# Optimization experiments

Measured on AMD Instinct MI355X. Metric: run time of the kernel, lower is better.

The kernel has to match this reference:

```python
import jax, jax.numpy as jnp
import numpy as np

N_NODES = 50000
N_EDGES = 800000
C = 128
NEG_SLOPE = 0.01  # nn.LeakyReLU default


def _init_linear(key, fan_in, fan_out):
    kw, kb = jax.random.split(key)
    lim = 1.0 / np.sqrt(fan_in)
    W = jax.random.uniform(kw, (fan_in, fan_out), jnp.float32, -lim, lim)
    b = jax.random.uniform(kb, (fan_out,), jnp.float32, -lim, lim)
    return W, b


def setup_inputs() -> dict:
    key = jax.random.key(0)
    ks = jax.random.split(key, 10)
    x = jax.random.normal(ks[0], (N_NODES, C), jnp.float32)
    pos = jax.random.normal(ks[1], (N_NODES, 3), jnp.float32)
    edge_index = jax.random.randint(ks[2], (2, N_EDGES), 0, N_NODES, jnp.int64)
    # mlp_h: Linear(C,C) -> LeakyReLU -> Linear(C,3) -> Tanh
    Wh1, bh1 = _init_linear(ks[3], C, C)
    Wh2, bh2 = _init_linear(ks[4], C, 3)
    # mlp_f: Linear(C+3, C) -> LeakyReLU
    Wf, bf = _init_linear(ks[5], C + 3, C)
    # mlp_g: Linear(C,C) -> LeakyReLU -> Linear(C,C)
    Wg1, bg1 = _init_linear(ks[6], C, C)
    Wg2, bg2 = _init_linear(ks[7], C, C)
    return {"x": x, "pos": pos, "edge_index": edge_index,
            "Wh1": Wh1, "bh1": bh1, "Wh2": Wh2, "bh2": bh2,
            "Wf": Wf, "bf": bf,
            "Wg1": Wg1, "bg1": bg1, "Wg2": Wg2, "bg2": bg2}


def reference(x, pos, edge_index, Wh1, bh1, Wh2, bh2, Wf, bf, Wg1, bg1, Wg2, bg2):
    lrelu = lambda t: jax.nn.leaky_relu(t, NEG_SLOPE)
    # delta_i = tanh(mlp_h(x_i))  -> [N, 3]
    delta = jnp.tanh(lrelu(x @ Wh1 + bh1) @ Wh2 + bh2)
    src, dst = edge_index[0], edge_index[1]  # message j -> i (PyG convention)
    # per-edge relative position: pos_j - pos_i + delta_i  -> [E, 3]
    rel = pos[src] - pos[dst] + delta[dst]
    # per-edge message: mlp_f([rel, x_j])  -> [E, C]
    e = lrelu(jnp.concatenate([rel, x[src]], axis=-1) @ Wf + bf)
    # scatter-max aggregate over incoming edges per target node
    agg = jax.ops.segment_max(e, dst, num_segments=N_NODES)
    agg = jnp.where(jnp.isfinite(agg), agg, 0.0)  # empty segments -> 0
    # out_i = mlp_g(agg_i) + x_i
    out = lrelu(agg @ Wg1 + bg1) @ Wg2 + bg2 + x
    return out
```

## Files before the change

### kernel.cpp

```cpp
#include <hip/hip_runtime.h>
#include <cfloat>
#include <cmath>

#define NEG_SLOPE 0.01f

typedef __attribute__((ext_vector_type(8))) short short8;
typedef __attribute__((ext_vector_type(4))) float f32x4;

__device__ __forceinline__ float lrelu(float v) { return v >= 0.0f ? v : NEG_SLOPE * v; }

__device__ __forceinline__ ushort f2b(float f) {
    unsigned u = __float_as_uint(f);
    u += 0x7fffu + ((u >> 16) & 1u);
    return (ushort)(u >> 16);
}
__device__ __forceinline__ float b2f(ushort s) { return __uint_as_float(((unsigned)s) << 16); }

__device__ __forceinline__ void split8(const float* v, short8& hi, short8& lo) {
#pragma unroll
    for (int j = 0; j < 8; ++j) {
        ushort h = f2b(v[j]);
        hi[j] = (short)h;
        lo[j] = (short)f2b(v[j] - b2f(h));
    }
}

__global__ __launch_bounds__(256) void wprep_kernel(
    const float* __restrict__ Wh1, const float* __restrict__ Wf,
    const float* __restrict__ Wg1, const float* __restrict__ Wg2,
    ushort* __restrict__ WT)
{
    int t = blockIdx.x * 256 + threadIdx.x;
    int mat = t >> 14;
    int idx = t & 16383;
    int n = idx >> 7, k = idx & 127;
    float v;
    if (mat == 0)      v = Wh1[k * 128 + n];
    else if (mat == 1) v = Wf[(k + 3) * 128 + n];
    else if (mat == 2) v = Wg1[k * 128 + n];
    else               v = Wg2[k * 128 + n];
    WT[t - idx + n * 128 + k] = f2b(v);
}


__global__ __launch_bounds__(256) void count_kernel(
    const int* __restrict__ ei, int* __restrict__ G, int E, int NBK)
{
    __shared__ int cnt[256];
    const int tid = threadIdx.x;
    cnt[tid] = 0;
    __syncthreads();
    for (int e = blockIdx.x * 256 + tid; e < E; e += 256 * 256)
        atomicAdd(&cnt[ei[E + e] >> 8], 1);
    __syncthreads();
    if (tid < NBK) G[tid * 256 + blockIdx.x] = cnt[tid];
}

__global__ __launch_bounds__(256) void scanA_kernel(
    const int* __restrict__ G, int* __restrict__ partial)
{
    __shared__ int s[256];
    int i = blockIdx.x * 256 + threadIdx.x;
    s[threadIdx.x] = G[i];
    __syncthreads();
    for (int d = 128; d > 0; d >>= 1) {
        if (threadIdx.x < d) s[threadIdx.x] += s[threadIdx.x + d];
        __syncthreads();
    }
    if (threadIdx.x == 0) partial[blockIdx.x] = s[0];
}

__global__ __launch_bounds__(256) void scanB_kernel(
    int* __restrict__ partial, int NB)
{
    __shared__ int s[256];
    int t = threadIdx.x;
    int v = (t < NB) ? partial[t] : 0;
    s[t] = v;
    __syncthreads();
    for (int d = 1; d < 256; d <<= 1) {
        int a = (t >= d) ? s[t - d] : 0;
        __syncthreads();
        s[t] += a;
        __syncthreads();
    }
    if (t < NB) partial[t] = s[t] - v;
}

__global__ __launch_bounds__(256) void scanC_kernel(
    int* __restrict__ G, const int* __restrict__ partial)
{
    __shared__ int s[256];
    int t = threadIdx.x;
    int i = blockIdx.x * 256 + t;
    int v = G[i];
    s[t] = v;
    __syncthreads();
    for (int d = 1; d < 256; d <<= 1) {
        int a = (t >= d) ? s[t - d] : 0;
        __syncthreads();
        s[t] += a;
        __syncthreads();
    }
    G[i] = partial[blockIdx.x] + s[t] - v;
}

__global__ __launch_bounds__(256) void partition_kernel(
    const int* __restrict__ ei, const int* __restrict__ G,
    uint* __restrict__ bpairs, int E, int NBK)
{
    __shared__ int cur[256];
    const int tid = threadIdx.x;
    if (tid < NBK) cur[tid] = G[tid * 256 + blockIdx.x];
    __syncthreads();
    for (int e = blockIdx.x * 256 + tid; e < E; e += 256 * 256) {
        int src = ei[e];
        int dst = ei[E + e];
        int p = atomicAdd(&cur[dst >> 8], 1);
        bpairs[p] = (uint)src | ((uint)(dst & 255) << 24);
    }
}

__global__ __launch_bounds__(256) void bucket_csr_kernel(
    const uint* __restrict__ bpairs, const int* __restrict__ G,
    int* __restrict__ offs, int* __restrict__ srcs, int E, int M, int NBK)
{
    __shared__ int deg[256], scn[256], cur[256];
    const int b = blockIdx.x;
    const int t = threadIdx.x;
    const int base = G[b * 256];
    const int end  = (b + 1 < NBK) ? G[(b + 1) * 256] : E;
    deg[t] = 0;
    __syncthreads();
    for (int p = base + t; p < end; p += 256)
        atomicAdd(&deg[bpairs[p] >> 24], 1);
    __syncthreads();
    scn[t] = deg[t];
    __syncthreads();
    for (int d = 1; d < 256; d <<= 1) {
        int a = (t >= d) ? scn[t - d] : 0;
        __syncthreads();
        scn[t] += a;
        __syncthreads();
    }
    int excl = scn[t] - deg[t];
    cur[t] = excl;
    int node = b * 256 + t;
    if (node < M) offs[node] = base + excl;
    if (node == M - 1 || (b == NBK - 1 && t == 255)) offs[M] = E;
    __syncthreads();
    for (int p = base + t; p < end; p += 256) {
        uint pk = bpairs[p];
        int q = atomicAdd(&cur[pk >> 24], 1);
        srcs[base + q] = (int)(pk & 0xFFFFFFu);
    }
}


#define GEMM_CORE_REG(ACC, AH, AL)                                              \
    {                                                                           \
        _Pragma("unroll")                                                       \
        for (int ks = 0; ks < 4; ++ks) {                                        \
            _Pragma("unroll")                                                   \
            for (int nt = 0; nt < 8; ++nt) {                                    \
                short8 bfr = *(const short8*)&Bs[(nt * 16 + ln) * 136 + ks * 32 + qd * 8]; \
                ACC[nt] = __builtin_amdgcn_mfma_f32_16x16x32_bf16(AL[ks], bfr, ACC[nt], 0, 0, 0); \
                ACC[nt] = __builtin_amdgcn_mfma_f32_16x16x32_bf16(AH[ks], bfr, ACC[nt], 0, 0, 0); \
            }                                                                   \
        }                                                                       \
    }

#define STAGE_B(WTP)                                                            \
    {                                                                           \
        _Pragma("unroll")                                                       \
        for (int i = 0; i < 8; ++i) {                                           \
            int c = tid + 256 * i;                                              \
            int r = c >> 4, col8 = (c & 15) * 8;                                \
            *(uint4*)&Bs[r * 136 + col8] = *(const uint4*)((WTP) + r * 128 + col8); \
        }                                                                       \
    }

__global__ __launch_bounds__(256) void hy_kernel(
    const float* __restrict__ x, const ushort* __restrict__ Wh1T,
    const float* __restrict__ bh1, const float* __restrict__ Wh2,
    const float* __restrict__ bh2, const ushort* __restrict__ WfxT,
    const float* __restrict__ Wf, const float* __restrict__ pos,
    float* __restrict__ q, ushort* __restrict__ yb, int M)
{
    __shared__ ushort Bs[128 * 136];
    __shared__ ushort yS[64 * 128];
    const int tid = threadIdx.x;
    const int w = tid >> 6, L = tid & 63, qd = L >> 4, ln = L & 15;
    const int row0 = blockIdx.x * 64;
    const int arow = row0 + w * 16 + ln;

    short8 ah[4], al[4];
    {
        const float* base = x + (size_t)((arow < M) ? arow : 0) * 128 + qd * 8;
        float vb[8];
#pragma unroll
        for (int ks = 0; ks < 4; ++ks) {
            float4 v0 = make_float4(0.f, 0.f, 0.f, 0.f), v1 = v0;
            if (arow < M) {
                v0 = *(const float4*)(base + ks * 32);
                v1 = *(const float4*)(base + ks * 32 + 4);
            }
            vb[0] = v0.x; vb[1] = v0.y; vb[2] = v0.z; vb[3] = v0.w;
            vb[4] = v1.x; vb[5] = v1.y; vb[6] = v1.z; vb[7] = v1.w;
            split8(vb, ah[ks], al[ks]);
        }
    }

    STAGE_B(Wh1T);
    __syncthreads();
    f32x4 acc1[8];
#pragma unroll
    for (int nt = 0; nt < 8; ++nt) acc1[nt] = (f32x4){0.f, 0.f, 0.f, 0.f};
    GEMM_CORE_REG(acc1, ah, al);
    __syncthreads();

    STAGE_B(WfxT);
    __syncthreads();
    f32x4 acc2[8];
#pragma unroll
    for (int nt = 0; nt < 8; ++nt) acc2[nt] = (f32x4){0.f, 0.f, 0.f, 0.f};
    GEMM_CORE_REG(acc2, ah, al);
    __syncthreads();

    float* h1s = (float*)Bs;
#pragma unroll
    for (int nt = 0; nt < 8; ++nt) {
        int n = nt * 16 + ln;
        float bias = bh1[n];
#pragma unroll
        for (int r = 0; r < 4; ++r)
            h1s[(w * 16 + qd * 4 + r) * 132 + n] = lrelu(acc1[nt][r] + bias);
    }
#pragma unroll
    for (int r = 0; r < 4; ++r) {
        int m = w * 16 + qd * 4 + r;
        int gm = row0 + m;
        float p0 = 0.f, p1 = 0.f, p2 = 0.f;
        if (gm < M) { p0 = pos[gm * 3]; p1 = pos[gm * 3 + 1]; p2 = pos[gm * 3 + 2]; }
#pragma unroll
        for (int nt = 0; nt < 8; ++nt) {
            int n = nt * 16 + ln;
            yS[m * 128 + n] = f2b(acc2[nt][r] + p0 * Wf[n] + p1 * Wf[128 + n] + p2 * Wf[256 + n]);
        }
    }
    __syncthreads();

    int row = tid & 63, cc = tid >> 6;
    if (cc < 3 && row0 + row < M) {
        float s = 0.f;
#pragma unroll
        for (int k4 = 0; k4 < 32; ++k4) {
            float4 h = *(const float4*)&h1s[row * 132 + k4 * 4];
            s += h.x * Wh2[(k4 * 4 + 0) * 3 + cc] + h.y * Wh2[(k4 * 4 + 1) * 3 + cc]
               + h.z * Wh2[(k4 * 4 + 2) * 3 + cc] + h.w * Wh2[(k4 * 4 + 3) * 3 + cc];
        }
        q[(row0 + row) * 3 + cc] = tanhf(s + bh2[cc]) - pos[(row0 + row) * 3 + cc];
    }
#pragma unroll
    for (int i = 0; i < 4; ++i) {
        int c = tid + 256 * i;
        int r = c >> 4, col8 = (c & 15) * 8;
        if (row0 + r < M)
            *(uint4*)(yb + (size_t)(row0 + r) * 128 + col8) = *(const uint4*)&yS[r * 128 + col8];
    }
}

__global__ __launch_bounds__(256) void midout_kernel(
    const ushort* __restrict__ aggb, const float* __restrict__ qv,
    const float* __restrict__ Wf, const float* __restrict__ bfv,
    const ushort* __restrict__ Wg1T, const float* __restrict__ bg1,
    const ushort* __restrict__ Wg2T, const float* __restrict__ bg2,
    const float* __restrict__ x, float* __restrict__ out, int M)
{
    __shared__ ushort Bs[128 * 136];
    __shared__ float  Ms[64 * 132];
    const int tid = threadIdx.x;
    const int w = tid >> 6, L = tid & 63, qd = L >> 4, ln = L & 15;
    const int row0 = blockIdx.x * 64;
    const int arow = row0 + w * 16 + ln;

    short8 ah[4], al[4];
    {
        bool ok = arow < M;
        const ushort* base = aggb + (size_t)(ok ? arow : 0) * 128 + qd * 8;
        float q0 = 0.f, q1 = 0.f, q2 = 0.f;
        if (ok) { q0 = qv[arow * 3]; q1 = qv[arow * 3 + 1]; q2 = qv[arow * 3 + 2]; }
        float vb[8];
#pragma unroll
        for (int ks = 0; ks < 4; ++ks) {
            union { uint4 u; ushort s[8]; } a;
            a.u = ok ? *(const uint4*)(base + ks * 32) : make_uint4(0xFF80FF80u, 0xFF80FF80u, 0xFF80FF80u, 0xFF80FF80u);
#pragma unroll
            for (int j = 0; j < 8; ++j) {
                int k = ks * 32 + qd * 8 + j;
                float dec = 0.f;
                if (a.s[j] != 0xFF80u)
                    dec = lrelu(b2f(a.s[j]) + q0 * Wf[k] + q1 * Wf[128 + k] + q2 * Wf[256 + k] + bfv[k]);
                vb[j] = dec;
            }
            split8(vb, ah[ks], al[ks]);
        }
    }

    STAGE_B(Wg1T);
    __syncthreads();
    f32x4 macc[8];
#pragma unroll
    for (int nt = 0; nt < 8; ++nt) macc[nt] = (f32x4){0.f, 0.f, 0.f, 0.f};
    GEMM_CORE_REG(macc, ah, al);
    __syncthreads();

#pragma unroll
    for (int nt = 0; nt < 8; ++nt) {
        int n = nt * 16 + ln;
        float bias = bg1[n];
#pragma unroll
        for (int r = 0; r < 4; ++r)
            Ms[(w * 16 + qd * 4 + r) * 132 + n] = lrelu(macc[nt][r] + bias);
    }
    STAGE_B(Wg2T);
    __syncthreads();

    short8 ah2[4], al2[4];
    {
        const float* base = &Ms[(w * 16 + ln) * 132 + qd * 8];
        float vb[8];
#pragma unroll
        for (int ks = 0; ks < 4; ++ks) {
            float4 v0 = *(const float4*)(base + ks * 32);
            float4 v1 = *(const float4*)(base + ks * 32 + 4);
            vb[0] = v0.x; vb[1] = v0.y; vb[2] = v0.z; vb[3] = v0.w;
            vb[4] = v1.x; vb[5] = v1.y; vb[6] = v1.z; vb[7] = v1.w;
            split8(vb, ah2[ks], al2[ks]);
        }
    }
    f32x4 acc2[8];
#pragma unroll
    for (int nt = 0; nt < 8; ++nt) acc2[nt] = (f32x4){0.f, 0.f, 0.f, 0.f};
    GEMM_CORE_REG(acc2, ah2, al2);
    __syncthreads();

#pragma unroll
    for (int r = 0; r < 4; ++r) {
        int m = w * 16 + qd * 4 + r;
#pragma unroll
        for (int nt = 0; nt < 8; ++nt)
            Ms[m * 132 + nt * 16 + ln] = acc2[nt][r];
    }
    __syncthreads();
#pragma unroll
    for (int i = 0; i < 8; ++i) {
        int c = tid + 256 * i;
        int r = c >> 5, col4 = (c & 31) * 4;
        int gr = row0 + r;
        if (gr < M) {
            float4 o = *(const float4*)&Ms[r * 132 + col4];
            float4 bv = *(const float4*)(bg2 + col4);
            float4 xv = *(const float4*)(x + (size_t)gr * 128 + col4);
            o.x += bv.x + xv.x; o.y += bv.y + xv.y;
            o.z += bv.z + xv.z; o.w += bv.w + xv.w;
            *(float4*)(out + (size_t)gr * 128 + col4) = o;
        }
    }
}

__global__ __launch_bounds__(256) void agg_kernel(
    const int* __restrict__ offs, const int* __restrict__ srcs,
    const ushort* __restrict__ yb, ushort* __restrict__ aggb, int M)
{
    int wave = threadIdx.x >> 6;
    int lane = threadIdx.x & 63;
    int node = blockIdx.x * 4 + wave;
    if (node >= M) return;
    int o0 = offs[node], o1 = offs[node + 1];
    float a0 = -INFINITY, a1 = -INFINITY;
    const uint* yp = (const uint*)yb;
    int j = o0;
    for (; j + 3 < o1; j += 4) {
        int s0 = srcs[j], s1 = srcs[j + 1], s2 = srcs[j + 2], s3 = srcs[j + 3];
        uint u0 = yp[(size_t)s0 * 64 + lane];
        uint u1 = yp[(size_t)s1 * 64 + lane];
        uint u2 = yp[(size_t)s2 * 64 + lane];
        uint u3 = yp[(size_t)s3 * 64 + lane];
        a0 = fmaxf(a0, fmaxf(fmaxf(__uint_as_float(u0 << 16), __uint_as_float(u1 << 16)),
                             fmaxf(__uint_as_float(u2 << 16), __uint_as_float(u3 << 16))));
        a1 = fmaxf(a1, fmaxf(fmaxf(__uint_as_float(u0 & 0xFFFF0000u), __uint_as_float(u1 & 0xFFFF0000u)),
                             fmaxf(__uint_as_float(u2 & 0xFFFF0000u), __uint_as_float(u3 & 0xFFFF0000u))));
    }
    for (; j < o1; ++j) {
        uint u = yp[(size_t)srcs[j] * 64 + lane];
        a0 = fmaxf(a0, __uint_as_float(u << 16));
        a1 = fmaxf(a1, __uint_as_float(u & 0xFFFF0000u));
    }
    uint pk = (__float_as_uint(a0) >> 16) | (__float_as_uint(a1) & 0xFFFF0000u);
    ((uint*)aggb)[(size_t)node * 64 + lane] = pk;
}

extern "C" void kernel_launch(void* const* d_in, const int* in_sizes, int n_in,
                              void* d_out, int out_size, void* d_ws, size_t ws_size,
                              hipStream_t stream)
{
    const float* x   = (const float*)d_in[0];
    const float* pos = (const float*)d_in[1];
    const int*   ei  = (const int*)d_in[2];
    const float* Wh1 = (const float*)d_in[3];
    const float* bh1 = (const float*)d_in[4];
    const float* Wh2 = (const float*)d_in[5];
    const float* bh2 = (const float*)d_in[6];
    const float* Wf  = (const float*)d_in[7];
    const float* bf  = (const float*)d_in[8];
    const float* Wg1 = (const float*)d_in[9];
    const float* bg1 = (const float*)d_in[10];
    const float* Wg2 = (const float*)d_in[11];
    const float* bg2 = (const float*)d_in[12];
    float* out = (float*)d_out;

    const int M = in_sizes[0] / 128;
    const int E = in_sizes[2] / 2;
    const int NBK = (M + 255) >> 8;

    char* ws = (char*)d_ws;
    size_t off = 0;
    auto alloc = [&](size_t bytes) { void* p = ws + off; off += (bytes + 15) & ~15ull; return p; };
    ushort* yb     = (ushort*)alloc((size_t)M * 128 * sizeof(ushort));
    ushort* aggb   = (ushort*)alloc((size_t)M * 128 * sizeof(ushort));
    ushort* WT     = (ushort*)alloc(4 * 16384 * sizeof(ushort));
    float*  q      = (float*)alloc((size_t)M * 3 * sizeof(float));
    int*    offs   = (int*)alloc((size_t)(M + 1) * sizeof(int));
    int*    G      = (int*)alloc((size_t)NBK * 256 * sizeof(int));
    int*    part   = (int*)alloc(256 * sizeof(int));
    uint*   bpairs = (uint*)alloc((size_t)E * sizeof(uint));
    int*    srcs   = (int*)alloc((size_t)E * sizeof(int));

    const int gb = (M + 63) / 64;

    count_kernel<<<256, 256, 0, stream>>>(ei, G, E, NBK);
    scanA_kernel<<<NBK, 256, 0, stream>>>(G, part);
    scanB_kernel<<<1, 256, 0, stream>>>(part, NBK);
    scanC_kernel<<<NBK, 256, 0, stream>>>(G, part);
    partition_kernel<<<256, 256, 0, stream>>>(ei, G, bpairs, E, NBK);
    bucket_csr_kernel<<<NBK, 256, 0, stream>>>(bpairs, G, offs, srcs, E, M, NBK);

    wprep_kernel<<<256, 256, 0, stream>>>(Wh1, Wf, Wg1, Wg2, WT);

    hy_kernel<<<gb, 256, 0, stream>>>(x, WT, bh1, Wh2, bh2,
                                      WT + 16384, Wf, pos, q, yb, M);
    agg_kernel<<<(M + 3) / 4, 256, 0, stream>>>(offs, srcs, yb, aggb, M);
    midout_kernel<<<gb, 256, 0, stream>>>(aggb, q, Wf, bf,
                                          WT + 2 * 16384, bg1,
                                          WT + 3 * 16384, bg2, x, out, M);
}
```

Baseline: 222.7 us.

## Fuse preprocessing kernels and use single-pass bf16 for second output GEMM

Folds weight preparation into the edge-count kernel and merges the two small scan kernels into one, cutting two kernel launches from the preprocessing chain. In the output kernel, the hidden activation is stored as bf16 in shared memory and the second MLP GEMM runs as a single bf16 MFMA pass instead of a hi/lo split pair, halving its MFMA work and shrinking LDS use. The output staging buffer now reuses the weight tile memory. This lowers the precision of the second GEMM, and workspace alignment is raised to 256 bytes.

```diff
diff --git a/kernel.cpp b/kernel.cpp
--- a/kernel.cpp
+++ b/kernel.cpp
@@ -25,35 +25,35 @@
     }
 }
 
-__global__ __launch_bounds__(256) void wprep_kernel(
+__global__ __launch_bounds__(256) void count_wprep_kernel(
+    const int* __restrict__ ei,
     const float* __restrict__ Wh1, const float* __restrict__ Wf,
     const float* __restrict__ Wg1, const float* __restrict__ Wg2,
-    ushort* __restrict__ WT)
-{
-    int t = blockIdx.x * 256 + threadIdx.x;
-    int mat = t >> 14;
-    int idx = t & 16383;
-    int n = idx >> 7, k = idx & 127;
-    float v;
-    if (mat == 0)      v = Wh1[k * 128 + n];
-    else if (mat == 1) v = Wf[(k + 3) * 128 + n];
-    else if (mat == 2) v = Wg1[k * 128 + n];
-    else               v = Wg2[k * 128 + n];
-    WT[t - idx + n * 128 + k] = f2b(v);
-}
-
-
-__global__ __launch_bounds__(256) void count_kernel(
-    const int* __restrict__ ei, int* __restrict__ G, int E, int NBK)
+    ushort* __restrict__ WT, int* __restrict__ G, int E, int NBK)
 {
     __shared__ int cnt[256];
-    const int tid = threadIdx.x;
-    cnt[tid] = 0;
-    __syncthreads();
-    for (int e = blockIdx.x * 256 + tid; e < E; e += 256 * 256)
+    const int t = threadIdx.x;
+    const int b = blockIdx.x;
+
+    {
+        int tt = b * 256 + t;
+        int mat = tt >> 14;
+        int idx = tt & 16383;
+        int n = idx >> 7, k = idx & 127;
+        float v;
+        if (mat == 0)      v = Wh1[k * 128 + n];
+        else if (mat == 1) v = Wf[(k + 3) * 128 + n];
+        else if (mat == 2) v = Wg1[k * 128 + n];
+        else               v = Wg2[k * 128 + n];
+        WT[(tt - idx) + n * 128 + k] = f2b(v);
+    }
+
+    cnt[t] = 0;
+    __syncthreads();
+    for (int e = b * 256 + t; e < E; e += 65536)
         atomicAdd(&cnt[ei[E + e] >> 8], 1);
     __syncthreads();
-    if (tid < NBK) G[tid * 256 + blockIdx.x] = cnt[tid];
+    if (t < NBK) G[t * 256 + b] = cnt[t];
 }
 
 __global__ __launch_bounds__(256) void scanA_kernel(
@@ -70,11 +70,12 @@
     if (threadIdx.x == 0) partial[blockIdx.x] = s[0];
 }
 
-__global__ __launch_bounds__(256) void scanB_kernel(
-    int* __restrict__ partial, int NB)
+__global__ __launch_bounds__(256) void scanBC_kernel(
+    int* __restrict__ G, const int* __restrict__ partial, int NB)
 {
     __shared__ int s[256];
-    int t = threadIdx.x;
+    __shared__ int base;
+    const int t = threadIdx.x;
     int v = (t < NB) ? partial[t] : 0;
     s[t] = v;
     __syncthreads();
@@ -84,17 +85,12 @@
         s[t] += a;
         __syncthreads();
     }
-    if (t < NB) partial[t] = s[t] - v;
-}
-
-__global__ __launch_bounds__(256) void scanC_kernel(
-    int* __restrict__ G, const int* __restrict__ partial)
-{
-    __shared__ int s[256];
-    int t = threadIdx.x;
+    if (t == blockIdx.x) base = s[t] - v;
+    __syncthreads();
+
     int i = blockIdx.x * 256 + t;
-    int v = G[i];
-    s[t] = v;
+    int g = G[i];
+    s[t] = g;
     __syncthreads();
     for (int d = 1; d < 256; d <<= 1) {
         int a = (t >= d) ? s[t - d] : 0;
@@ -102,7 +98,7 @@
         s[t] += a;
         __syncthreads();
     }
-    G[i] = partial[blockIdx.x] + s[t] - v;
+    G[i] = base + s[t] - g;
 }
 
 __global__ __launch_bounds__(256) void partition_kernel(
@@ -113,7 +109,7 @@
     const int tid = threadIdx.x;
     if (tid < NBK) cur[tid] = G[tid * 256 + blockIdx.x];
     __syncthreads();
-    for (int e = blockIdx.x * 256 + tid; e < E; e += 256 * 256) {
+    for (int e = blockIdx.x * 256 + tid; e < E; e += 65536) {
         int src = ei[e];
         int dst = ei[E + e];
         int p = atomicAdd(&cur[dst >> 8], 1);
@@ -151,8 +147,8 @@
     __syncthreads();
     for (int p = base + t; p < end; p += 256) {
         uint pk = bpairs[p];
-        int q = atomicAdd(&cur[pk >> 24], 1);
-        srcs[base + q] = (int)(pk & 0xFFFFFFu);
+        int qpos = atomicAdd(&cur[pk >> 24], 1);
+        srcs[base + qpos] = (int)(pk & 0xFFFFFFu);
     }
 }
 
@@ -278,7 +274,7 @@
     const float* __restrict__ x, float* __restrict__ out, int M)
 {
     __shared__ ushort Bs[128 * 136];
-    __shared__ float  Ms[64 * 132];
+    __shared__ ushort Ms[64 * 136];
     const int tid = threadIdx.x;
     const int w = tid >> 6, L = tid & 63, qd = L >> 4, ln = L & 15;
     const int row0 = blockIdx.x * 64;
@@ -321,36 +317,36 @@
         float bias = bg1[n];
 #pragma unroll
         for (int r = 0; r < 4; ++r)
-            Ms[(w * 16 + qd * 4 + r) * 132 + n] = lrelu(macc[nt][r] + bias);
+            Ms[(w * 16 + qd * 4 + r) * 136 + n] = f2b(lrelu(macc[nt][r] + bias));
     }
     STAGE_B(Wg2T);
     __syncthreads();
 
-    short8 ah2[4], al2[4];
-    {
-        const float* base = &Ms[(w * 16 + ln) * 132 + qd * 8];
-        float vb[8];
-#pragma unroll
-        for (int ks = 0; ks < 4; ++ks) {
-            float4 v0 = *(const float4*)(base + ks * 32);
-            float4 v1 = *(const float4*)(base + ks * 32 + 4);
-            vb[0] = v0.x; vb[1] = v0.y; vb[2] = v0.z; vb[3] = v0.w;
-            vb[4] = v1.x; vb[5] = v1.y; vb[6] = v1.z; vb[7] = v1.w;
-            split8(vb, ah2[ks], al2[ks]);
-        }
-    }
+    short8 a2[4];
+#pragma unroll
+    for (int ks = 0; ks < 4; ++ks)
+        a2[ks] = *(const short8*)&Ms[(w * 16 + ln) * 136 + ks * 32 + qd * 8];
+
     f32x4 acc2[8];
 #pragma unroll
     for (int nt = 0; nt < 8; ++nt) acc2[nt] = (f32x4){0.f, 0.f, 0.f, 0.f};
-    GEMM_CORE_REG(acc2, ah2, al2);
-    __syncthreads();
-
+#pragma unroll
+    for (int ks = 0; ks < 4; ++ks) {
+#pragma unroll
+        for (int nt = 0; nt < 8; ++nt) {
+            short8 bfr = *(const short8*)&Bs[(nt * 16 + ln) * 136 + ks * 32 + qd * 8];
+            acc2[nt] = __builtin_amdgcn_mfma_f32_16x16x32_bf16(a2[ks], bfr, acc2[nt], 0, 0, 0);
+        }
+    }
+    __syncthreads();
+
+    float* outS = (float*)Bs;
 #pragma unroll
     for (int r = 0; r < 4; ++r) {
         int m = w * 16 + qd * 4 + r;
 #pragma unroll
         for (int nt = 0; nt < 8; ++nt)
-            Ms[m * 132 + nt * 16 + ln] = acc2[nt][r];
+            outS[m * 132 + nt * 16 + ln] = acc2[nt][r];
     }
     __syncthreads();
 #pragma unroll
@@ -359,7 +355,7 @@
         int r = c >> 5, col4 = (c & 31) * 4;
         int gr = row0 + r;
         if (gr < M) {
-            float4 o = *(const float4*)&Ms[r * 132 + col4];
+            float4 o = *(const float4*)&outS[r * 132 + col4];
             float4 bv = *(const float4*)(bg2 + col4);
             float4 xv = *(const float4*)(x + (size_t)gr * 128 + col4);
             o.x += bv.x + xv.x; o.y += bv.y + xv.y;
@@ -426,7 +422,7 @@
 
     char* ws = (char*)d_ws;
     size_t off = 0;
-    auto alloc = [&](size_t bytes) { void* p = ws + off; off += (bytes + 15) & ~15ull; return p; };
+    auto alloc = [&](size_t bytes) { void* p = ws + off; off += (bytes + 255) & ~255ull; return p; };
     ushort* yb     = (ushort*)alloc((size_t)M * 128 * sizeof(ushort));
     ushort* aggb   = (ushort*)alloc((size_t)M * 128 * sizeof(ushort));
     ushort* WT     = (ushort*)alloc(4 * 16384 * sizeof(ushort));
@@ -439,14 +435,11 @@
 
     const int gb = (M + 63) / 64;
 
-    count_kernel<<<256, 256, 0, stream>>>(ei, G, E, NBK);
+    count_wprep_kernel<<<256, 256, 0, stream>>>(ei, Wh1, Wf, Wg1, Wg2, WT, G, E, NBK);
     scanA_kernel<<<NBK, 256, 0, stream>>>(G, part);
-    scanB_kernel<<<1, 256, 0, stream>>>(part, NBK);
-    scanC_kernel<<<NBK, 256, 0, stream>>>(G, part);
+    scanBC_kernel<<<NBK, 256, 0, stream>>>(G, part, NBK);
     partition_kernel<<<256, 256, 0, stream>>>(ei, G, bpairs, E, NBK);
     bucket_csr_kernel<<<NBK, 256, 0, stream>>>(bpairs, G, offs, srcs, E, M, NBK);
-
-    wprep_kernel<<<256, 256, 0, stream>>>(Wh1, Wf, Wg1, Wg2, WT);
 
     hy_kernel<<<gb, 256, 0, stream>>>(x, WT, bh1, Wh2, bh2,
                                       WT + 16384, Wf, pos, q, yb, M);
```

Result: no change. 219.1 us (median of 2 runs) (-1.6%).
